# Kernel optimization log

Hardware: AMD Instinct MI355X
Metric: run time of the kernel (lower is better)

The kernel has to match this reference:

```python
import jax, jax.numpy as jnp
import numpy as np

STRIDES = (8, 16, 32, 64)
NUM_HEADS = 8
G = 4
P = 32
TAU_Z = 2.0
LVL_BASE = 3.0  # stride 8 == 2**3 maps to level 0


def decode_box(xyzr):
    scale = jnp.exp2(xyzr[..., 2:3])
    ratio = jnp.exp2(jnp.concatenate([-0.5 * xyzr[..., 3:4], 0.5 * xyzr[..., 3:4]], axis=-1))
    wh = scale * ratio
    xy = xyzr[..., 0:2]
    return jnp.concatenate([xy - 0.5 * wh, xy + 0.5 * wh], axis=-1)


def position_embedding(box, num_feats, temperature=10000.0):
    term = jnp.array([1000.0, 1000.0, 1.0, 1.0], dtype=box.dtype)
    token = box / term
    dim_t = jnp.arange(num_feats, dtype=jnp.float32)
    dim_t = temperature ** (2.0 * (dim_t // 2) / num_feats)
    pos = token[..., None] / dim_t  # B,N,4,F
    pos = jnp.stack([jnp.sin(pos[..., 0::2]), jnp.cos(pos[..., 1::2])], axis=4)
    B, N = box.shape[:2]
    return pos.reshape(B, N, -1)  # B,N,4*F


def bbox_iof(boxes):
    # boxes: B,N,4 x1y1x2y2; iof[b,i,j] = inter(i,j) / area(i)
    area = jnp.clip(boxes[..., 2] - boxes[..., 0], 0.0) * jnp.clip(boxes[..., 3] - boxes[..., 1], 0.0)
    lt = jnp.maximum(boxes[:, :, None, :2], boxes[:, None, :, :2])
    rb = jnp.minimum(boxes[:, :, None, 2:], boxes[:, None, :, 2:])
    wh = jnp.clip(rb - lt, 0.0)
    inter = wh[..., 0] * wh[..., 1]
    return inter / jnp.clip(area[:, :, None], 1e-7, None)


def bilinear_group_sample(feat, xy, stride):
    # feat: [B,C,H,W]; xy: [B,N,P,G,2] image coords -> [B,N,G,P,C//G]
    B, C, H, W = feat.shape
    _, N, Pn, Gn, _ = xy.shape
    Cg = C // Gn
    featg = feat.reshape(B, Gn, Cg, H * W).transpose(0, 1, 3, 2)  # B,G,HW,Cg
    px = xy[..., 0] / stride - 0.5  # grid_sample align_corners=False convention
    py = xy[..., 1] / stride - 0.5
    x0 = jnp.floor(px)
    y0 = jnp.floor(py)
    bi = jnp.arange(B)[:, None, None]
    gi = jnp.arange(Gn)[None, :, None]
    out = jnp.zeros((B, Gn, N * Pn, Cg), dtype=feat.dtype)
    for dx in (0.0, 1.0):
        for dy in (0.0, 1.0):
            xi = x0 + dx
            yi = y0 + dy
            wgt = (1.0 - jnp.abs(px - xi)) * (1.0 - jnp.abs(py - yi))
            valid = (xi >= 0) & (xi <= W - 1) & (yi >= 0) & (yi <= H - 1)
            wgt = wgt * valid  # zero padding outside
            xi_c = jnp.clip(xi, 0, W - 1).astype(jnp.int32)
            yi_c = jnp.clip(yi, 0, H - 1).astype(jnp.int32)
            idx = (yi_c * W + xi_c).transpose(0, 3, 1, 2).reshape(B, Gn, N * Pn)
            vals = featg[bi, gi, idx]  # B,G,N*P,Cg
            w = wgt.transpose(0, 3, 1, 2).reshape(B, Gn, N * Pn, 1)
            out = out + vals * w
    return out.reshape(B, Gn, N, Pn, Cg).transpose(0, 2, 1, 3, 4)


def layer_norm(x, g, b, eps=1e-5):
    mu = jnp.mean(x, axis=-1, keepdims=True)
    var = jnp.mean((x - mu) ** 2, axis=-1, keepdims=True)
    return (x - mu) * jax.lax.rsqrt(var + eps) * g + b


def _forward(feats, query_content, query_box, Wq, bq, Wk, bk, Wv, bv, Wo, bo,
             ln_g, ln_b, off_W, off_b, sc_W, sc_b, iof_tau):
    B, N, C = query_content.shape
    H = NUM_HEADS
    dh = C // H
    box_cxcy = query_box[..., :2]
    zc = query_box[..., 2:3]
    rc = query_box[..., 3:4]
    box_wh = jnp.exp2(zc) * jnp.exp2(jnp.concatenate([-0.5 * rc, 0.5 * rc], axis=-1))
    logscale = zc.reshape(B, N, 1, 1)

    # torch.no_grad() block -> stop_gradient
    rois = decode_box(query_box)
    iof = jnp.log(bbox_iof(jax.lax.stop_gradient(rois)) + 1e-7)  # B,N,N
    pe = jax.lax.stop_gradient(position_embedding(query_box, C // 4))  # B,N,C
    attn_bias = iof[:, None, :, :] * iof_tau.reshape(1, -1, 1, 1)  # B,H,N,N

    x = query_content + pe
    q = (x @ Wq.T + bq).reshape(B, N, H, dh)
    k = (x @ Wk.T + bk).reshape(B, N, H, dh)
    v = (x @ Wv.T + bv).reshape(B, N, H, dh)
    scores = jnp.einsum('bnhd,bmhd->bhnm', q, k) * (dh ** -0.5) + attn_bias
    attn = jax.nn.softmax(scores, axis=-1)
    ctx = jnp.einsum('bhnm,bmhd->bnhd', attn, v).reshape(B, N, C)
    qc = x + ctx @ Wo.T + bo  # mmcv MultiheadAttention adds identity (= query+pe)
    qc = layer_norm(qc, ln_g, ln_b)

    offset = (qc @ off_W.T + off_b).reshape(B, N, P, G, 2)
    scale_logit = (qc @ sc_W.T + sc_b).reshape(B, N, P, G)
    sample_xy = box_cxcy.reshape(B, N, 1, 1, 2) + offset * box_wh.reshape(B, N, 1, 1, 2)
    sample_z = scale_logit + logscale  # B,N,P,G
    lvl = sample_z - LVL_BASE
    levels = jnp.arange(len(STRIDES), dtype=jnp.float32)
    zw = jax.nn.softmax(-((lvl[..., None] - levels) ** 2) / TAU_Z, axis=-1)  # B,N,P,G,L
    zw_t = zw.transpose(0, 1, 3, 2, 4)  # B,N,G,P,L
    sample_feats = jnp.zeros(())
    for l, (fm, s) in enumerate(zip(feats, STRIDES)):
        sample_feats = sample_feats + bilinear_group_sample(fm, sample_xy, s) * zw_t[..., l:l + 1]
    return sample_feats, sample_xy, offset, sample_z, scale_logit, qc


def setup_inputs():
    key = jax.random.key(0)
    ks = jax.random.split(key, 20)
    B, N, C = 4, 500, 256
    feat0 = jax.random.normal(ks[0], (B, C, 128, 128), dtype=jnp.float32)
    feat1 = jax.random.normal(ks[1], (B, C, 64, 64), dtype=jnp.float32)
    feat2 = jax.random.normal(ks[2], (B, C, 32, 32), dtype=jnp.float32)
    feat3 = jax.random.normal(ks[3], (B, C, 16, 16), dtype=jnp.float32)
    query_content = jax.random.normal(ks[4], (B, N, C), dtype=jnp.float32)
    xy = jax.random.uniform(ks[5], (B, N, 2), minval=64.0, maxval=960.0)
    zz = jax.random.uniform(ks[6], (B, N, 1), minval=3.0, maxval=6.0)
    rr = jax.random.uniform(ks[7], (B, N, 1), minval=-1.0, maxval=1.0)
    query_box = jnp.concatenate([xy, zz, rr], axis=-1)
    sub_query_xy = jax.random.normal(ks[8], (B, N, P, G, 2), dtype=jnp.float32) * 0.1
    sub_query_z = jax.random.normal(ks[9], (B, N, P, G, 4), dtype=jnp.float32) * 0.1
    sub_query_vec = jax.random.normal(ks[10], (B, N, P, G, 64), dtype=jnp.float32) * 0.1
    imgs_whwh = jnp.full((B, N, 4), 1024.0, dtype=jnp.float32)
    w = lambda i, sh: jax.random.normal(ks[i], sh, dtype=jnp.float32) * 0.02
    return {
        'feat0': feat0, 'feat1': feat1, 'feat2': feat2, 'feat3': feat3,
        'query_content': query_content, 'query_box': query_box,
        'sub_query_xy': sub_query_xy, 'sub_query_z': sub_query_z,
        'sub_query_vec': sub_query_vec, 'imgs_whwh': imgs_whwh,
        'Wq': w(11, (C, C)), 'bq': jnp.zeros((C,), jnp.float32),
        'Wk': w(12, (C, C)), 'bk': jnp.zeros((C,), jnp.float32),
        'Wv': w(13, (C, C)), 'bv': jnp.zeros((C,), jnp.float32),
        'Wo': w(14, (C, C)), 'bo': jnp.zeros((C,), jnp.float32),
        'ln_g': jnp.ones((C,), jnp.float32), 'ln_b': jnp.zeros((C,), jnp.float32),
        'off_W': w(15, (2 * G * P, C)),
        'off_b': jax.random.uniform(ks[16], (2 * G * P,), minval=-0.5, maxval=0.5),
        'sc_W': w(17, (G * P, C)),
        'sc_b': jax.random.normal(ks[18], (G * P,), dtype=jnp.float32) * 0.1,
        'iof_tau': jax.random.uniform(ks[19], (NUM_HEADS,), minval=0.0, maxval=4.0),
    }


def reference(feat0, feat1, feat2, feat3, query_content, query_box, sub_query_xy,
              sub_query_z, sub_query_vec, imgs_whwh, Wq, bq, Wk, bk, Wv, bv, Wo, bo,
              ln_g, ln_b, off_W, off_b, sc_W, sc_b, iof_tau):
    sample_feats, sample_xy, offset, sample_z, scale_logit, qc = _forward(
        [feat0, feat1, feat2, feat3], query_content, query_box,
        Wq, bq, Wk, bk, Wv, bv, Wo, bo, ln_g, ln_b, off_W, off_b, sc_W, sc_b, iof_tau)
    return (sample_feats, sub_query_xy, sub_query_z, sub_query_vec, qc,
            sample_xy, offset, sample_z, scale_logit)
```

## Files before the change

### kernel.cpp

```cpp
#include <hip/hip_runtime.h>
#include <cstdint>
#include <cstddef>

#define B_ 4
#define N_ 500
#define C_ 256
#define NH_ 8
#define DH_ 32
#define P_ 32
#define G_ 4
#define CG_ 64
#define BN_ (B_*N_)
#define QKV_QI 8

__constant__ const int LVL_W[4] = {128, 64, 32, 16};

static __device__ __forceinline__ unsigned short f2bf(float f) {
  union { float f; unsigned u; } v; v.f = f;
  unsigned r = v.u + 0x7FFF + ((v.u >> 16) & 1);
  return (unsigned short)(r >> 16);
}
static __device__ __forceinline__ float bf2f(unsigned u16shifted) {
  union { unsigned u; float f; } v; v.u = u16shifted;
  return v.f;
}

__global__ __launch_bounds__(256) void mega_kernel(
    const float* __restrict__ f0, const float* __restrict__ f1,
    const float* __restrict__ f2, const float* __restrict__ f3,
    unsigned short* __restrict__ t0, unsigned short* __restrict__ t1,
    unsigned short* __restrict__ t2, unsigned short* __restrict__ t3) {
  __shared__ unsigned short tile[64][260];
  int blk = blockIdx.x;
  int t = threadIdx.x;
  const float* src; unsigned short* dst; int npix, i;
  if (blk < 1024)      { src = f0; dst = t0; npix = 16384; i = blk; }
  else if (blk < 1280) { src = f1; dst = t1; npix = 4096;  i = blk - 1024; }
  else if (blk < 1344) { src = f2; dst = t2; npix = 1024;  i = blk - 1280; }
  else                 { src = f3; dst = t3; npix = 256;   i = blk - 1344; }
  int pb = npix >> 8;
  int px0 = (i % pb) * 256;
  int c0 = ((i / pb) & 3) * 64;
  int b  = i / (pb * 4);
  int lane = t & 63;
  int wv = t >> 6;
#pragma unroll
  for (int k = 0; k < 16; k++) {
    int r = k * 4 + wv;
    float4 v = *(const float4*)&src[((size_t)b * C_ + c0 + r) * npix + px0 + lane * 4];
    ushort4 u;
    u.x = f2bf(v.x); u.y = f2bf(v.y); u.z = f2bf(v.z); u.w = f2bf(v.w);
    int col = (lane * 4) ^ (((r >> 4) & 3) << 2);
    *(ushort4*)&tile[r][col] = u;
  }
  __syncthreads();
  int cq = t & 15;
  int pr = t >> 4;
#pragma unroll
  for (int k = 0; k < 16; k++) {
    int p = k * 16 + pr;
    ushort4 r4;
    {
      int ch = cq * 4;
      r4.x = tile[ch + 0][p ^ ((((ch + 0) >> 4) & 3) << 2)];
      r4.y = tile[ch + 1][p ^ ((((ch + 1) >> 4) & 3) << 2)];
      r4.z = tile[ch + 2][p ^ ((((ch + 2) >> 4) & 3) << 2)];
      r4.w = tile[ch + 3][p ^ ((((ch + 3) >> 4) & 3) << 2)];
    }
    *(ushort4*)&dst[((size_t)b * npix + px0 + p) * C_ + c0 + cq * 4] = r4;
  }
}

__global__ __launch_bounds__(256) void qkv_prep_kernel(
    const float* __restrict__ qcontent, const float* __restrict__ qbox,
    const float* __restrict__ Wq, const float* __restrict__ bq,
    const float* __restrict__ Wk, const float* __restrict__ bk,
    const float* __restrict__ Wv, const float* __restrict__ bv,
    float* __restrict__ x, float* __restrict__ boxd,
    float* __restrict__ q, float* __restrict__ kT, float* __restrict__ v) {
  __shared__ float xs[QKV_QI][C_];
  int blk = blockIdx.x;
  int t = threadIdx.x;
  int bn0 = blk * QKV_QI;
  int d = t >> 6;
  float tj = exp2f((float)((t >> 1) & 31) * 0.4152410f);
  float tmul = (d < 2) ? 0.001f : 1.0f;
  for (int i = 0; i < QKV_QI; i++) {
    float qv = qbox[(size_t)(bn0 + i) * 4 + d];
    float val = qv * tmul / tj;
    float pe = (t & 1) ? cosf(val) : sinf(val);
    float xv = qcontent[(size_t)(bn0 + i) * C_ + t] + pe;
    xs[i][t] = xv;
    x[(size_t)(bn0 + i) * C_ + t] = xv;
  }
  if (t < QKV_QI) {
    int bn = bn0 + t;
    const float* qb = qbox + (size_t)bn * 4;
    float cx = qb[0], cy = qb[1], z = qb[2], r = qb[3];
    float scale = exp2f(z);
    float w = scale * exp2f(-0.5f * r);
    float h = scale * exp2f(0.5f * r);
    float* bd = boxd + (size_t)bn * 12;
    float x1 = cx - 0.5f * w, y1 = cy - 0.5f * h, x2 = cx + 0.5f * w, y2 = cy + 0.5f * h;
    bd[0] = x1; bd[1] = y1; bd[2] = x2; bd[3] = y2;
    bd[4] = cx; bd[5] = cy; bd[6] = w; bd[7] = h; bd[8] = z;
    float area = fmaxf(x2 - x1, 0.f) * fmaxf(y2 - y1, 0.f);
    bd[9] = fmaxf(area, 1e-7f);
  }
  __syncthreads();
  float accq[QKV_QI], acck[QKV_QI], accv[QKV_QI];
  for (int i = 0; i < QKV_QI; i++) { accq[i] = 0.f; acck[i] = 0.f; accv[i] = 0.f; }
  const float4* wq4 = (const float4*)(Wq + (size_t)t * C_);
  const float4* wk4 = (const float4*)(Wk + (size_t)t * C_);
  const float4* wv4 = (const float4*)(Wv + (size_t)t * C_);
  for (int k4 = 0; k4 < C_ / 4; k4++) {
    float4 wq = wq4[k4], wk = wk4[k4], wv = wv4[k4];
    for (int i = 0; i < QKV_QI; i++) {
      float4 xv = *(const float4*)&xs[i][k4 * 4];
      accq[i] += xv.x * wq.x + xv.y * wq.y + xv.z * wq.z + xv.w * wq.w;
      acck[i] += xv.x * wk.x + xv.y * wk.y + xv.z * wk.z + xv.w * wk.w;
      accv[i] += xv.x * wv.x + xv.y * wv.y + xv.z * wv.z + xv.w * wv.w;
    }
  }
  for (int i = 0; i < QKV_QI; i++) {
    int bn = bn0 + i;
    int b = bn / N_;
    int n = bn % N_;
    q[(size_t)bn * C_ + t] = accq[i] + bq[t];
    kT[((size_t)b * C_ + t) * N_ + n] = acck[i] + bk[t];
    v[(size_t)bn * C_ + t] = accv[i] + bv[t];
  }
}

__global__ __launch_bounds__(256) void score_copy_kernel(
    const float* __restrict__ q, const float* __restrict__ kT,
    const float* __restrict__ boxd, const float* __restrict__ tau_p,
    float* __restrict__ S, float* __restrict__ Mpart,
    const float* __restrict__ subxy, const float* __restrict__ subz,
    const float* __restrict__ subv,
    float* __restrict__ o_subxy, float* __restrict__ o_subz,
    float* __restrict__ o_subv) {
  int blk = blockIdx.x;
  int t = threadIdx.x;
  if (blk >= 512) {
    int cb = blk - 512;
    const float4* s4; float4* d4;
    if (cb < 125)      { s4 = (const float4*)subxy + (size_t)cb * 1024;
                         d4 = (float4*)o_subxy + (size_t)cb * 1024; }
    else if (cb < 375) { s4 = (const float4*)subz + (size_t)(cb - 125) * 1024;
                         d4 = (float4*)o_subz + (size_t)(cb - 125) * 1024; }
    else               { s4 = (const float4*)subv + (size_t)(cb - 375) * 1024;
                         d4 = (float4*)o_subv + (size_t)(cb - 375) * 1024; }
    d4[t] = s4[t];
    d4[t + 256] = s4[t + 256];
    d4[t + 512] = s4[t + 512];
    d4[t + 768] = s4[t + 768];
    return;
  }
  int mp = (blk >> 1) & 7;
  int npar = blk & 1;
  int h = (blk >> 4) & 7;
  int b = blk >> 7;
  int w = t >> 6;
  int lane = t & 63;
  int m = mp * 64 + lane;
  int mc = min(m, N_ - 1);
  bool mok = m < N_;
  float tau = tau_p[h];
  const float scl = 0.17677669529663687f;

  float kreg[DH_];
  const float* kbase = kT + ((size_t)b * C_ + h * DH_) * N_ + mc;
#pragma unroll
  for (int d = 0; d < DH_; d++) kreg[d] = kbase[(size_t)d * N_];

  const float* bm = boxd + ((size_t)b * N_ + mc) * 12;
  float kx1 = bm[0], ky1 = bm[1], kx2 = bm[2], ky2 = bm[3];

  size_t srow_base = ((size_t)(b * NH_ + h)) * N_;
  for (int n = npar * 4 + w; n < N_; n += 8) {
    const float* qn = q + ((size_t)b * N_ + n) * C_ + h * DH_;
    float4 q0 = *(const float4*)&qn[0];
    float4 q1 = *(const float4*)&qn[4];
    float4 q2 = *(const float4*)&qn[8];
    float4 q3 = *(const float4*)&qn[12];
    float4 q4 = *(const float4*)&qn[16];
    float4 q5 = *(const float4*)&qn[20];
    float4 q6 = *(const float4*)&qn[24];
    float4 q7 = *(const float4*)&qn[28];
    float s0 = q0.x*kreg[0] + q0.y*kreg[1] + q0.z*kreg[2] + q0.w*kreg[3];
    float s1 = q1.x*kreg[4] + q1.y*kreg[5] + q1.z*kreg[6] + q1.w*kreg[7];
    float s2 = q2.x*kreg[8] + q2.y*kreg[9] + q2.z*kreg[10] + q2.w*kreg[11];
    float s3 = q3.x*kreg[12] + q3.y*kreg[13] + q3.z*kreg[14] + q3.w*kreg[15];
    s0 += q4.x*kreg[16] + q4.y*kreg[17] + q4.z*kreg[18] + q4.w*kreg[19];
    s1 += q5.x*kreg[20] + q5.y*kreg[21] + q5.z*kreg[22] + q5.w*kreg[23];
    s2 += q6.x*kreg[24] + q6.y*kreg[25] + q6.z*kreg[26] + q6.w*kreg[27];
    s3 += q7.x*kreg[28] + q7.y*kreg[29] + q7.z*kreg[30] + q7.w*kreg[31];
    float s = (s0 + s1) + (s2 + s3);

    const float* bn = boxd + ((size_t)b * N_ + n) * 12;
    float4 nb = *(const float4*)&bn[0];
    float inv_area = 1.0f / bn[9];
    float iw = fmaxf(fminf(nb.z, kx2) - fmaxf(nb.x, kx1), 0.f);
    float ih = fmaxf(fminf(nb.w, ky2) - fmaxf(nb.y, ky1), 0.f);
    float bias = logf(iw * ih * inv_area + 1e-7f);
    float sc = s * scl + bias * tau;

    if (mok) S[(srow_base + n) * 512 + m] = sc;
    float wm = mok ? sc : -1e30f;
#pragma unroll
    for (int off = 32; off >= 1; off >>= 1) wm = fmaxf(wm, __shfl_xor(wm, off, 64));
    if (lane == 0) Mpart[(srow_base + n) * 8 + mp] = wm;
  }
}

__global__ __launch_bounds__(256) void pv_kernel2(
    const float* __restrict__ S, const float* __restrict__ Mpart,
    const float* __restrict__ v, float* __restrict__ ctx) {
  __shared__ float pl[4][512];
  __shared__ float red[4][4];
  int t = threadIdx.x;
  int n0 = blockIdx.x * 4;
  int h = blockIdx.y;
  int b = blockIdx.z;
  size_t rb = ((size_t)(b * NH_ + h)) * N_;

  float mx[4];
#pragma unroll
  for (int qq = 0; qq < 4; qq++) {
    const float* mp = Mpart + (rb + n0 + qq) * 8;
    float m0 = fmaxf(fmaxf(mp[0], mp[1]), fmaxf(mp[2], mp[3]));
    float m1 = fmaxf(fmaxf(mp[4], mp[5]), fmaxf(mp[6], mp[7]));
    mx[qq] = fmaxf(m0, m1);
  }
  float psum[4];
#pragma unroll
  for (int qq = 0; qq < 4; qq++) {
    const float* Srow = S + (rb + n0 + qq) * 512;
    float e0 = (t < N_) ? __expf(Srow[min(t, N_ - 1)] - mx[qq]) : 0.f;
    int m1i = t + 256;
    float e1 = (m1i < N_) ? __expf(Srow[min(m1i, N_ - 1)] - mx[qq]) : 0.f;
    pl[qq][t] = e0;
    pl[qq][t + 256] = e1;
    psum[qq] = e0 + e1;
  }
  int wv = t >> 6, lane = t & 63;
#pragma unroll
  for (int qq = 0; qq < 4; qq++) {
    float s = psum[qq];
#pragma unroll
    for (int off = 32; off >= 1; off >>= 1) s += __shfl_xor(s, off, 64);
    if (lane == 0) red[qq][wv] = s;
  }
  __syncthreads();

  int c = lane & 31;
  int mh = lane >> 5;
  const float* vb = v + ((size_t)b * N_) * C_ + h * DH_ + c;
  const float* prow = pl[wv];
  int mstart = mh ? 252 : 0;
  int mend = mh ? 500 : 252;
  float a0 = 0.f, a1 = 0.f, a2 = 0.f, a3 = 0.f;
  for (int m = mstart; m < mend; m += 4) {
    float p0 = prow[m], p1 = prow[m + 1], p2 = prow[m + 2], p3 = prow[m + 3];
    a0 += p0 * vb[(size_t)m * C_];
    a1 += p1 * vb[(size_t)(m + 1) * C_];
    a2 += p2 * vb[(size_t)(m + 2) * C_];
    a3 += p3 * vb[(size_t)(m + 3) * C_];
  }
  float a = (a0 + a1) + (a2 + a3);
  a += __shfl_xor(a, 32, 64);
  if (mh == 0) {
    float inv = 1.0f / (red[wv][0] + red[wv][1] + red[wv][2] + red[wv][3]);
    ctx[((size_t)b * N_ + n0 + wv) * C_ + h * DH_ + c] = a * inv;
  }
}

#define PQI 4
__global__ __launch_bounds__(256) void projln_head_kernel(
    const float* __restrict__ ctx, const float* __restrict__ x,
    const float* __restrict__ Wo, const float* __restrict__ bo,
    const float* __restrict__ ln_g, const float* __restrict__ ln_b,
    const float* __restrict__ boxd,
    const float* __restrict__ offW, const float* __restrict__ offb,
    const float* __restrict__ scW, const float* __restrict__ scb,
    float* __restrict__ qc_out,
    float* __restrict__ out_offset, float* __restrict__ out_sxy,
    float* __restrict__ out_sz, float* __restrict__ out_sl,
    float* __restrict__ zw_ws) {
  __shared__ float cs[PQI][C_];
  __shared__ float qs[PQI][C_];
  __shared__ float redbuf[PQI][8];
  int blk = blockIdx.x;
  int t = threadIdx.x;
  int bn0 = blk * PQI;
  for (int i = 0; i < PQI; i++) cs[i][t] = ctx[(size_t)(bn0 + i) * C_ + t];
  __syncthreads();
  float acc[PQI] = {0.f, 0.f, 0.f, 0.f};
  {
    const float4* w4 = (const float4*)(Wo + (size_t)t * C_);
    for (int k4 = 0; k4 < C_ / 4; k4++) {
      float4 w = w4[k4];
      for (int i = 0; i < PQI; i++) {
        float4 cv = *(const float4*)&cs[i][k4 * 4];
        acc[i] += cv.x * w.x + cv.y * w.y + cv.z * w.z + cv.w * w.w;
      }
    }
  }
  float y[PQI];
  int wave = t >> 6, lane = t & 63;
  for (int i = 0; i < PQI; i++) {
    y[i] = x[(size_t)(bn0 + i) * C_ + t] + acc[i] + bo[t];
    float s1 = y[i], s2 = y[i] * y[i];
#pragma unroll
    for (int off = 32; off >= 1; off >>= 1) {
      s1 += __shfl_xor(s1, off, 64);
      s2 += __shfl_xor(s2, off, 64);
    }
    if (lane == 0) { redbuf[i][wave] = s1; redbuf[i][wave + 4] = s2; }
  }
  __syncthreads();
  for (int i = 0; i < PQI; i++) {
    float s1 = redbuf[i][0] + redbuf[i][1] + redbuf[i][2] + redbuf[i][3];
    float s2 = redbuf[i][4] + redbuf[i][5] + redbuf[i][6] + redbuf[i][7];
    float mu = s1 * (1.0f / C_);
    float var = s2 * (1.0f / C_) - mu * mu;
    float inv = rsqrtf(var + 1e-5f);
    float o = (y[i] - mu) * inv * ln_g[t] + ln_b[t];
    qs[i][t] = o;
    qc_out[(size_t)(bn0 + i) * C_ + t] = o;
  }
  __syncthreads();
  float ao[PQI] = {0.f, 0.f, 0.f, 0.f};
  {
    const float4* w4 = (const float4*)(offW + (size_t)t * C_);
    for (int k4 = 0; k4 < C_ / 4; k4++) {
      float4 w = w4[k4];
      for (int i = 0; i < PQI; i++) {
        float4 cv = *(const float4*)&qs[i][k4 * 4];
        ao[i] += cv.x * w.x + cv.y * w.y + cv.z * w.z + cv.w * w.w;
      }
    }
  }
  int xy = t & 1;
  for (int i = 0; i < PQI; i++) {
    int bn = bn0 + i;
    const float* bd = boxd + (size_t)bn * 12;
    float off = ao[i] + offb[t];
    float ctr = xy ? bd[5] : bd[4];
    float wh = xy ? bd[7] : bd[6];
    float sxy = ctr + off * wh;
    out_offset[(size_t)bn * 256 + t] = off;
    out_sxy[(size_t)bn * 256 + t] = sxy;
  }
  if (t < 128) {
    float as[PQI] = {0.f, 0.f, 0.f, 0.f};
    const float4* sw4 = (const float4*)(scW + (size_t)t * C_);
    for (int k4 = 0; k4 < C_ / 4; k4++) {
      float4 w = sw4[k4];
      for (int i = 0; i < PQI; i++) {
        float4 cv = *(const float4*)&qs[i][k4 * 4];
        as[i] += cv.x * w.x + cv.y * w.y + cv.z * w.z + cv.w * w.w;
      }
    }
    for (int i = 0; i < PQI; i++) {
      int bn = bn0 + i;
      const float* bd = boxd + (size_t)bn * 12;
      float sl = as[i] + scb[t];
      float sz = sl + bd[8];
      out_sl[(size_t)bn * 128 + t] = sl;
      out_sz[(size_t)bn * 128 + t] = sz;
      float lvl = sz - 3.0f;
      float d1 = lvl - 1.f, d2 = lvl - 2.f, d3 = lvl - 3.f;
      float e0 = __expf(-0.5f * lvl * lvl);
      float e1 = __expf(-0.5f * d1 * d1);
      float e2 = __expf(-0.5f * d2 * d2);
      float e3 = __expf(-0.5f * d3 * d3);
      float inv = 1.0f / (e0 + e1 + e2 + e3);
      float* zw = zw_ws + ((size_t)bn * 128 + t) * 4;
      zw[0] = e0 * inv; zw[1] = e1 * inv; zw[2] = e2 * inv; zw[3] = e3 * inv;
    }
  }
}

__global__ __launch_bounds__(256) void sample_kernel_v4(
    const unsigned short* __restrict__ f0, const unsigned short* __restrict__ f1,
    const unsigned short* __restrict__ f2, const unsigned short* __restrict__ f3,
    const float* __restrict__ sxy, const float* __restrict__ zw_ws,
    float* __restrict__ out) {
  int t = threadIdx.x;
  int wv = t >> 6;
  int lane = t & 63;
  int sub = lane >> 3;
  int c8 = lane & 7;
  int pt = blockIdx.x * 32 + wv * 8 + sub;
  int g = pt & 3;
  int p = (pt >> 2) & 31;
  int bn = pt >> 7;
  int b = bn / N_;

  float sx = sxy[(size_t)pt * 2];
  float sy = sxy[(size_t)pt * 2 + 1];
  const float* zw = zw_ws + (size_t)pt * 4;
  const unsigned short* feats[4] = {f0, f1, f2, f3};
  const float inv_stride[4] = {0.125f, 0.0625f, 0.03125f, 0.015625f};
  float acc0 = 0.f, acc1 = 0.f, acc2 = 0.f, acc3 = 0.f;
  float acc4 = 0.f, acc5 = 0.f, acc6 = 0.f, acc7 = 0.f;
#pragma unroll
  for (int l = 0; l < 4; l++) {
    float wl = zw[l];
    int W = LVL_W[l];
    float px = sx * inv_stride[l] - 0.5f;
    float py = sy * inv_stride[l] - 0.5f;
    float x0f = floorf(px), y0f = floorf(py);
    float fx = px - x0f, fy = py - y0f;
    int x0 = (int)x0f, y0 = (int)y0f;
    const unsigned short* fb = feats[l] + (size_t)b * W * W * C_ + g * CG_ + c8 * 8;
#pragma unroll
    for (int dy = 0; dy < 2; dy++) {
#pragma unroll
      for (int dx = 0; dx < 2; dx++) {
        int xi = x0 + dx, yi = y0 + dy;
        float valid = (xi >= 0 && xi < W && yi >= 0 && yi < W) ? 1.f : 0.f;
        int xc = min(max(xi, 0), W - 1);
        int yc = min(max(yi, 0), W - 1);
        float wgt = (dx ? fx : 1.f - fx) * (dy ? fy : 1.f - fy) * valid * wl;
        uint4 u = *(const uint4*)&fb[((size_t)yc * W + xc) * C_];
        acc0 += wgt * bf2f(u.x << 16);
        acc1 += wgt * bf2f(u.x & 0xFFFF0000u);
        acc2 += wgt * bf2f(u.y << 16);
        acc3 += wgt * bf2f(u.y & 0xFFFF0000u);
        acc4 += wgt * bf2f(u.z << 16);
        acc5 += wgt * bf2f(u.z & 0xFFFF0000u);
        acc6 += wgt * bf2f(u.w << 16);
        acc7 += wgt * bf2f(u.w & 0xFFFF0000u);
      }
    }
  }
  float* ob = &out[(size_t)bn * 8192 + g * 2048 + p * 64 + c8 * 8];
  float4 o0 = {acc0, acc1, acc2, acc3};
  float4 o1 = {acc4, acc5, acc6, acc7};
  *(float4*)&ob[0] = o0;
  *(float4*)&ob[4] = o1;
}

__global__ __launch_bounds__(256) void sample_kernel_native(
    const float* __restrict__ f0, const float* __restrict__ f1,
    const float* __restrict__ f2, const float* __restrict__ f3,
    const float* __restrict__ sxy, const float* __restrict__ zw_ws,
    float* __restrict__ out) {
  int t = threadIdx.x;
  int wv = t >> 6;
  int lane = t & 63;
  int pt = blockIdx.x * 4 + wv;
  int g = pt & 3;
  int p = (pt >> 2) & 31;
  int bn = pt >> 7;
  int b = bn / N_;
  float sx = sxy[(size_t)pt * 2];
  float sy = sxy[(size_t)pt * 2 + 1];
  const float* zw = zw_ws + (size_t)pt * 4;
  const float* feats[4] = {f0, f1, f2, f3};
  const float inv_stride[4] = {0.125f, 0.0625f, 0.03125f, 0.015625f};
  float acc = 0.f;
#pragma unroll
  for (int l = 0; l < 4; l++) {
    float wl = zw[l];
    int W = LVL_W[l];
    float px = sx * inv_stride[l] - 0.5f;
    float py = sy * inv_stride[l] - 0.5f;
    float x0f = floorf(px), y0f = floorf(py);
    float fx = px - x0f, fy = py - y0f;
    int x0 = (int)x0f, y0 = (int)y0f;
#pragma unroll
    for (int dy = 0; dy < 2; dy++) {
#pragma unroll
      for (int dx = 0; dx < 2; dx++) {
        int xi = x0 + dx, yi = y0 + dy;
        if (xi >= 0 && xi < W && yi >= 0 && yi < W) {
          float wgt = (dx ? fx : 1.f - fx) * (dy ? fy : 1.f - fy);
          float v = feats[l][(((size_t)b * C_ + g * CG_ + lane) * W + yi) * W + xi];
          acc += wgt * wl * v;
        }
      }
    }
  }
  out[(size_t)bn * 8192 + g * 2048 + p * 64 + lane] = acc;
}

extern "C" void kernel_launch(void* const* d_in, const int* in_sizes, int n_in,
                              void* d_out, int out_size, void* d_ws, size_t ws_size,
                              hipStream_t stream) {
  (void)in_sizes; (void)n_in; (void)out_size;
  const float* feat[4] = {(const float*)d_in[0], (const float*)d_in[1],
                          (const float*)d_in[2], (const float*)d_in[3]};
  const float* query_content = (const float*)d_in[4];
  const float* query_box = (const float*)d_in[5];
  const float* Wq = (const float*)d_in[10]; const float* bq = (const float*)d_in[11];
  const float* Wk = (const float*)d_in[12]; const float* bk = (const float*)d_in[13];
  const float* Wv = (const float*)d_in[14]; const float* bv = (const float*)d_in[15];
  const float* Wo = (const float*)d_in[16]; const float* bo = (const float*)d_in[17];
  const float* ln_g = (const float*)d_in[18]; const float* ln_b = (const float*)d_in[19];
  const float* offW = (const float*)d_in[20]; const float* offb = (const float*)d_in[21];
  const float* scW = (const float*)d_in[22]; const float* scb = (const float*)d_in[23];
  const float* iof_tau = (const float*)d_in[24];

  float* out = (float*)d_out;
  float* ws = (float*)d_ws;

  const size_t O_FEATS = 0;
  const size_t O_SUBXY = 16384000;
  const size_t O_SUBZ = 16896000;
  const size_t O_SUBV = 17920000;
  const size_t O_QC = 34304000;
  const size_t O_SXY = 34816000;
  const size_t O_OFF = 35328000;
  const size_t O_SZ = 35840000;
  const size_t O_SL = 36096000;

  float* S = out + O_FEATS;
  float* Mpart = out + O_FEATS + 8192000;

  const size_t o_x = 0;
  const size_t o_boxd = o_x + 512000;
  const size_t o_q = o_boxd + 24000;
  const size_t o_kT = o_q + 512000;
  const size_t o_v = o_kT + 512000;
  const size_t o_ctx = o_v + 512000;
  const size_t o_zw = o_ctx + 512000;
  const size_t o_ft = o_zw + 1024000;
  const size_t ft_sz[4] = {16777216, 4194304, 1048576, 262144};
  const size_t ft_total = ft_sz[0] + ft_sz[1] + ft_sz[2] + ft_sz[3];
  const size_t need_T = o_ft * sizeof(float) + ft_total * sizeof(unsigned short);
  const bool useT = ws_size >= need_T;

  unsigned short* ftu = (unsigned short*)(ws + o_ft);
  unsigned short* ftb[4] = {ftu,
                            ftu + ft_sz[0],
                            ftu + ft_sz[0] + ft_sz[1],
                            ftu + ft_sz[0] + ft_sz[1] + ft_sz[2]};

  if (useT) {
    mega_kernel<<<1360, 256, 0, stream>>>(
        feat[0], feat[1], feat[2], feat[3],
        ftb[0], ftb[1], ftb[2], ftb[3]);
  }

  qkv_prep_kernel<<<BN_ / QKV_QI, 256, 0, stream>>>(
      query_content, query_box, Wq, bq, Wk, bk, Wv, bv,
      ws + o_x, ws + o_boxd, ws + o_q, ws + o_kT, ws + o_v);

  score_copy_kernel<<<512 + 4375, 256, 0, stream>>>(
      ws + o_q, ws + o_kT, ws + o_boxd, iof_tau, S, Mpart,
      (const float*)d_in[6], (const float*)d_in[7], (const float*)d_in[8],
      out + O_SUBXY, out + O_SUBZ, out + O_SUBV);

  {
    dim3 gb(N_ / 4, NH_, B_);
    pv_kernel2<<<gb, 256, 0, stream>>>(S, Mpart, ws + o_v, ws + o_ctx);
  }

  projln_head_kernel<<<BN_ / PQI, 256, 0, stream>>>(
      ws + o_ctx, ws + o_x, Wo, bo, ln_g, ln_b, ws + o_boxd,
      offW, offb, scW, scb,
      out + O_QC, out + O_OFF, out + O_SXY, out + O_SZ, out + O_SL,
      ws + o_zw);

  const int npoints = BN_ * P_ * G_;
  if (useT) {
    sample_kernel_v4<<<npoints / 32, 256, 0, stream>>>(
        ftb[0], ftb[1], ftb[2], ftb[3],
        out + O_SXY, ws + o_zw, out + O_FEATS);
  } else {
    sample_kernel_native<<<npoints / 4, 256, 0, stream>>>(
        feat[0], feat[1], feat[2], feat[3],
        out + O_SXY, ws + o_zw, out + O_FEATS);
  }
}
```

Measured before the change: 291.2 us.

## Fuse score computation and softmax-PV into one attention kernel

Merges the score kernel and the PV kernel into a single attention kernel. Each block computes scores for 4 queries against all keys directly into shared memory, then does the softmax max/sum and the PV product. This removes the global round trip of the full score matrix and the partial-max buffer, plus one kernel launch. In exchange, each block now rereads the K columns for its query group, so K traffic rises by roughly 125x per (b,h), though it should mostly hit in cache.

```diff
diff --git a/kernel.cpp b/kernel.cpp
--- a/kernel.cpp
+++ b/kernel.cpp
@@ -132,18 +132,23 @@
   }
 }
 
-__global__ __launch_bounds__(256) void score_copy_kernel(
+__global__ __launch_bounds__(256) void attn_copy_kernel(
     const float* __restrict__ q, const float* __restrict__ kT,
-    const float* __restrict__ boxd, const float* __restrict__ tau_p,
-    float* __restrict__ S, float* __restrict__ Mpart,
+    const float* __restrict__ v, const float* __restrict__ boxd,
+    const float* __restrict__ tau_p, float* __restrict__ ctx,
     const float* __restrict__ subxy, const float* __restrict__ subz,
     const float* __restrict__ subv,
     float* __restrict__ o_subxy, float* __restrict__ o_subz,
     float* __restrict__ o_subv) {
+  __shared__ float pl[4][512];
+  __shared__ float qs[4][DH_];
+  __shared__ float qb5[4][5];
+  __shared__ float redm[4][4];
+  __shared__ float reds[4][4];
   int blk = blockIdx.x;
   int t = threadIdx.x;
-  if (blk >= 512) {
-    int cb = blk - 512;
+  if (blk >= 4000) {
+    int cb = blk - 4000;
     const float4* s4; float4* d4;
     if (cb < 125)      { s4 = (const float4*)subxy + (size_t)cb * 1024;
                          d4 = (float4*)o_subxy + (size_t)cb * 1024; }
@@ -157,100 +162,79 @@
     d4[t + 768] = s4[t + 768];
     return;
   }
-  int mp = (blk >> 1) & 7;
-  int npar = blk & 1;
-  int h = (blk >> 4) & 7;
-  int b = blk >> 7;
-  int w = t >> 6;
-  int lane = t & 63;
-  int m = mp * 64 + lane;
-  int mc = min(m, N_ - 1);
-  bool mok = m < N_;
+  int n0 = (blk % 125) * 4;
+  int bh = blk / 125;
+  int h = bh & 7;
+  int b = bh >> 3;
+
+  if (t < 128) {
+    int qq = t >> 5, dd = t & 31;
+    qs[qq][dd] = q[((size_t)b * N_ + n0 + qq) * C_ + h * DH_ + dd];
+  }
+  if (t < 4) {
+    const float* bd = boxd + ((size_t)b * N_ + n0 + t) * 12;
+    qb5[t][0] = bd[0]; qb5[t][1] = bd[1]; qb5[t][2] = bd[2]; qb5[t][3] = bd[3];
+    qb5[t][4] = 1.0f / bd[9];
+  }
+  __syncthreads();
+
   float tau = tau_p[h];
   const float scl = 0.17677669529663687f;
-
-  float kreg[DH_];
-  const float* kbase = kT + ((size_t)b * C_ + h * DH_) * N_ + mc;
-#pragma unroll
-  for (int d = 0; d < DH_; d++) kreg[d] = kbase[(size_t)d * N_];
-
-  const float* bm = boxd + ((size_t)b * N_ + mc) * 12;
-  float kx1 = bm[0], ky1 = bm[1], kx2 = bm[2], ky2 = bm[3];
-
-  size_t srow_base = ((size_t)(b * NH_ + h)) * N_;
-  for (int n = npar * 4 + w; n < N_; n += 8) {
-    const float* qn = q + ((size_t)b * N_ + n) * C_ + h * DH_;
-    float4 q0 = *(const float4*)&qn[0];
-    float4 q1 = *(const float4*)&qn[4];
-    float4 q2 = *(const float4*)&qn[8];
-    float4 q3 = *(const float4*)&qn[12];
-    float4 q4 = *(const float4*)&qn[16];
-    float4 q5 = *(const float4*)&qn[20];
-    float4 q6 = *(const float4*)&qn[24];
-    float4 q7 = *(const float4*)&qn[28];
-    float s0 = q0.x*kreg[0] + q0.y*kreg[1] + q0.z*kreg[2] + q0.w*kreg[3];
-    float s1 = q1.x*kreg[4] + q1.y*kreg[5] + q1.z*kreg[6] + q1.w*kreg[7];
-    float s2 = q2.x*kreg[8] + q2.y*kreg[9] + q2.z*kreg[10] + q2.w*kreg[11];
-    float s3 = q3.x*kreg[12] + q3.y*kreg[13] + q3.z*kreg[14] + q3.w*kreg[15];
-    s0 += q4.x*kreg[16] + q4.y*kreg[17] + q4.z*kreg[18] + q4.w*kreg[19];
-    s1 += q5.x*kreg[20] + q5.y*kreg[21] + q5.z*kreg[22] + q5.w*kreg[23];
-    s2 += q6.x*kreg[24] + q6.y*kreg[25] + q6.z*kreg[26] + q6.w*kreg[27];
-    s3 += q7.x*kreg[28] + q7.y*kreg[29] + q7.z*kreg[30] + q7.w*kreg[31];
-    float s = (s0 + s1) + (s2 + s3);
-
-    const float* bn = boxd + ((size_t)b * N_ + n) * 12;
-    float4 nb = *(const float4*)&bn[0];
-    float inv_area = 1.0f / bn[9];
-    float iw = fmaxf(fminf(nb.z, kx2) - fmaxf(nb.x, kx1), 0.f);
-    float ih = fmaxf(fminf(nb.w, ky2) - fmaxf(nb.y, ky1), 0.f);
-    float bias = logf(iw * ih * inv_area + 1e-7f);
-    float sc = s * scl + bias * tau;
-
-    if (mok) S[(srow_base + n) * 512 + m] = sc;
-    float wm = mok ? sc : -1e30f;
-#pragma unroll
-    for (int off = 32; off >= 1; off >>= 1) wm = fmaxf(wm, __shfl_xor(wm, off, 64));
-    if (lane == 0) Mpart[(srow_base + n) * 8 + mp] = wm;
-  }
-}
-
-__global__ __launch_bounds__(256) void pv_kernel2(
-    const float* __restrict__ S, const float* __restrict__ Mpart,
-    const float* __restrict__ v, float* __restrict__ ctx) {
-  __shared__ float pl[4][512];
-  __shared__ float red[4][4];
-  int t = threadIdx.x;
-  int n0 = blockIdx.x * 4;
-  int h = blockIdx.y;
-  int b = blockIdx.z;
-  size_t rb = ((size_t)(b * NH_ + h)) * N_;
-
+  float tmax[4] = {-1e30f, -1e30f, -1e30f, -1e30f};
+
+#pragma unroll
+  for (int half = 0; half < 2; half++) {
+    int m = t + half * 256;
+    int mc = min(m, N_ - 1);
+    bool ok = m < N_;
+    const float* kb = kT + ((size_t)b * C_ + h * DH_) * N_ + mc;
+    float s[4] = {0.f, 0.f, 0.f, 0.f};
+#pragma unroll
+    for (int d = 0; d < DH_; d++) {
+      float kd = kb[(size_t)d * N_];
+#pragma unroll
+      for (int qq = 0; qq < 4; qq++) s[qq] += qs[qq][d] * kd;
+    }
+    const float* bm = boxd + ((size_t)b * N_ + mc) * 12;
+    float kx1 = bm[0], ky1 = bm[1], kx2 = bm[2], ky2 = bm[3];
+#pragma unroll
+    for (int qq = 0; qq < 4; qq++) {
+      float iw = fmaxf(fminf(qb5[qq][2], kx2) - fmaxf(qb5[qq][0], kx1), 0.f);
+      float ih = fmaxf(fminf(qb5[qq][3], ky2) - fmaxf(qb5[qq][1], ky1), 0.f);
+      float bias = logf(iw * ih * qb5[qq][4] + 1e-7f);
+      float sc = ok ? (s[qq] * scl + bias * tau) : -1e30f;
+      pl[qq][t + half * 256] = sc;
+      tmax[qq] = fmaxf(tmax[qq], sc);
+    }
+  }
+  int wv = t >> 6, lane = t & 63;
+#pragma unroll
+  for (int qq = 0; qq < 4; qq++) {
+    float tm = tmax[qq];
+#pragma unroll
+    for (int off = 32; off >= 1; off >>= 1) tm = fmaxf(tm, __shfl_xor(tm, off, 64));
+    if (lane == 0) redm[qq][wv] = tm;
+  }
+  __syncthreads();
   float mx[4];
 #pragma unroll
+  for (int qq = 0; qq < 4; qq++)
+    mx[qq] = fmaxf(fmaxf(redm[qq][0], redm[qq][1]), fmaxf(redm[qq][2], redm[qq][3]));
+  float psum[4];
+#pragma unroll
   for (int qq = 0; qq < 4; qq++) {
-    const float* mp = Mpart + (rb + n0 + qq) * 8;
-    float m0 = fmaxf(fmaxf(mp[0], mp[1]), fmaxf(mp[2], mp[3]));
-    float m1 = fmaxf(fmaxf(mp[4], mp[5]), fmaxf(mp[6], mp[7]));
-    mx[qq] = fmaxf(m0, m1);
-  }
-  float psum[4];
-#pragma unroll
-  for (int qq = 0; qq < 4; qq++) {
-    const float* Srow = S + (rb + n0 + qq) * 512;
-    float e0 = (t < N_) ? __expf(Srow[min(t, N_ - 1)] - mx[qq]) : 0.f;
-    int m1i = t + 256;
-    float e1 = (m1i < N_) ? __expf(Srow[min(m1i, N_ - 1)] - mx[qq]) : 0.f;
+    float e0 = __expf(pl[qq][t] - mx[qq]);
+    float e1 = __expf(pl[qq][t + 256] - mx[qq]);
     pl[qq][t] = e0;
     pl[qq][t + 256] = e1;
     psum[qq] = e0 + e1;
   }
-  int wv = t >> 6, lane = t & 63;
 #pragma unroll
   for (int qq = 0; qq < 4; qq++) {
     float s = psum[qq];
 #pragma unroll
     for (int off = 32; off >= 1; off >>= 1) s += __shfl_xor(s, off, 64);
-    if (lane == 0) red[qq][wv] = s;
+    if (lane == 0) reds[qq][wv] = s;
   }
   __syncthreads();
 
@@ -271,7 +255,7 @@
   float a = (a0 + a1) + (a2 + a3);
   a += __shfl_xor(a, 32, 64);
   if (mh == 0) {
-    float inv = 1.0f / (red[wv][0] + red[wv][1] + red[wv][2] + red[wv][3]);
+    float inv = 1.0f / (reds[wv][0] + reds[wv][1] + reds[wv][2] + reds[wv][3]);
     ctx[((size_t)b * N_ + n0 + wv) * C_ + h * DH_ + c] = a * inv;
   }
 }
@@ -518,9 +502,6 @@
   const size_t O_SZ = 35840000;
   const size_t O_SL = 36096000;
 
-  float* S = out + O_FEATS;
-  float* Mpart = out + O_FEATS + 8192000;
-
   const size_t o_x = 0;
   const size_t o_boxd = o_x + 512000;
   const size_t o_q = o_boxd + 24000;
@@ -550,15 +531,10 @@
       query_content, query_box, Wq, bq, Wk, bk, Wv, bv,
       ws + o_x, ws + o_boxd, ws + o_q, ws + o_kT, ws + o_v);
 
-  score_copy_kernel<<<512 + 4375, 256, 0, stream>>>(
-      ws + o_q, ws + o_kT, ws + o_boxd, iof_tau, S, Mpart,
+  attn_copy_kernel<<<4000 + 4375, 256, 0, stream>>>(
+      ws + o_q, ws + o_kT, ws + o_v, ws + o_boxd, iof_tau, ws + o_ctx,
       (const float*)d_in[6], (const float*)d_in[7], (const float*)d_in[8],
       out + O_SUBXY, out + O_SUBZ, out + O_SUBV);
-
-  {
-    dim3 gb(N_ / 4, NH_, B_);
-    pv_kernel2<<<gb, 256, 0, stream>>>(S, Mpart, ws + o_v, ws + o_ctx);
-  }
 
   projln_head_kernel<<<BN_ / PQI, 256, 0, stream>>>(
       ws + o_ctx, ws + o_x, Wo, bo, ln_g, ln_b, ws + o_boxd,
```

Result: faster. 274.4 us (-5.8%).
